# Performance work log

Measured on AMD Instinct MI355X. Metric: run time of the kernel, lower is better.

Reference implementation:

```python
import jax, jax.numpy as jnp
import numpy as np

MAX_THRESHOLD = 0.25  # init kwarg
B, S, D, E = 8, 4096, 512, 8


def setup_inputs() -> dict:
    key = jax.random.key(0)
    ks = jax.random.split(key, 5)
    scale = 1.0 / np.sqrt(D)
    return {
        "inputs": jax.random.normal(ks[0], (B, S, D), dtype=jnp.float32),
        "W_gate": jax.random.normal(ks[1], (D, E), dtype=jnp.float32) * scale,
        "b_gate": jnp.zeros((E,), dtype=jnp.float32),
        "W_thr": jax.random.normal(ks[2], (D, 1), dtype=jnp.float32) * scale,
        "b_thr": jnp.zeros((1,), dtype=jnp.float32),
        "W_exp": jax.random.normal(ks[3], (E, D, D), dtype=jnp.float32) * scale,
        "b_exp": jnp.zeros((E, D), dtype=jnp.float32),
    }


def reference(inputs, W_gate, b_gate, W_thr, b_thr, W_exp, b_exp):
    d = inputs.shape[-1]
    x = inputs.reshape(-1, d)  # [T, D]
    # gating
    gate_logits = jax.nn.softmax(x @ W_gate + b_gate, axis=-1)          # [T, E]
    thresholds = jax.nn.sigmoid(x @ W_thr + b_thr) * MAX_THRESHOLD      # [T, 1]
    adapted = gate_logits - thresholds                                  # [T, E]
    selected = (adapted >= 0).astype(x.dtype)                           # [T, E]
    weights = adapted * selected                                        # [T, E]
    wsum = jnp.sum(weights, axis=-1, keepdims=True)
    wsum = jnp.where(wsum == 0, jnp.ones_like(wsum), wsum)
    weights = weights / wsum
    # dense-equivalent of gather->expert->scatter (weights are 0 where unselected)
    ex_out = jnp.einsum('td,edf->etf', x, W_exp) + b_exp[:, None, :]    # [E, T, D]
    results = jnp.einsum('etf,te->tf', ex_out, weights)                 # [T, D]
    return results.reshape(inputs.shape[:-1] + (results.shape[-1],))
```

## Files before the change

### kernel.cpp

```cpp
#include <hip/hip_runtime.h>


#define T_TOKENS 32768
#define DDIM 512
#define KDIM 4096
#define SLOTB 16384
#define SLOTA 16384

typedef __attribute__((ext_vector_type(8))) short short8;
typedef __attribute__((ext_vector_type(4))) float floatx4;
typedef __bf16 bf16x2 __attribute__((ext_vector_type(2)));

__device__ __forceinline__ unsigned short f2bf(float f) {
    unsigned int u = __float_as_uint(f);
    u += 0x7FFFu + ((u >> 16) & 1u);
    return (unsigned short)(u >> 16);
}

__device__ __forceinline__ unsigned int pk2(float a, float b) {
#if __has_builtin(__builtin_amdgcn_cvt_pk_bf16_f32)
    bf16x2 v = __builtin_amdgcn_cvt_pk_bf16_f32(a, b);
    return __builtin_bit_cast(unsigned int, v);
#else
    return (unsigned int)f2bf(a) | ((unsigned int)f2bf(b) << 16);
#endif
}

__device__ __forceinline__ void async_copy16(const void* g, void* l) {
    __builtin_amdgcn_global_load_lds(
        (const __attribute__((address_space(1))) void*)g,
        (__attribute__((address_space(3))) void*)l, 16, 0, 0);
}

__device__ __forceinline__ unsigned int scale_pair(unsigned int u, float w) {
    float lo = __uint_as_float(u << 16) * w;
    float hi = __uint_as_float(u & 0xFFFF0000u) * w;
    return pk2(lo, hi);
}

__global__ __launch_bounds__(256) void gating_cvt_bt(
    const float* __restrict__ x, const float* __restrict__ Wg,
    const float* __restrict__ bg, const float* __restrict__ Wt,
    const float* __restrict__ bt, float* __restrict__ wbuf,
    unsigned short* __restrict__ Xbf,
    const float* __restrict__ Wexp, unsigned short* __restrict__ Bt)
{
    __shared__ float sW[512 * 12];
    const int tid = threadIdx.x;

    if (blockIdx.x >= 512) {
        float(*tile)[65] = (float(*)[65])sW;
        const int bb = blockIdx.x - 512;
        const int k0 = (bb & 63) * 64;
        const int n0 = (bb >> 6) * 64;
        const int r = tid >> 4, cq = tid & 15;
#pragma unroll
        for (int p = 0; p < 4; ++p) {
            const int rr = p * 16 + r;
            const float4 v = *(const float4*)(Wexp + (size_t)(k0 + rr) * 512 + n0 + cq * 4);
            tile[rr][cq * 4 + 0] = v.x;
            tile[rr][cq * 4 + 1] = v.y;
            tile[rr][cq * 4 + 2] = v.z;
            tile[rr][cq * 4 + 3] = v.w;
        }
        __syncthreads();
        const int rn = tid >> 2;
        const int kq = tid & 3;
        alignas(16) unsigned short buf[16];
#pragma unroll
        for (int j = 0; j < 16; ++j) buf[j] = f2bf(tile[kq * 16 + j][rn]);
        unsigned short* dst = Bt + (size_t)(n0 + rn) * KDIM + k0 + kq * 16;
        *(uint4*)(dst) = *(const uint4*)(buf);
        *(uint4*)(dst + 8) = *(const uint4*)(buf + 8);
        return;
    }

    for (int i = tid; i < 512 * 9; i += 256) {
        int d = i / 9, e = i - d * 9;
        sW[d * 12 + e] = (e < 8) ? Wg[d * 8 + e] : Wt[d];
    }
    __syncthreads();

    const int t = blockIdx.x * 64 + (tid >> 2);
    const int q = tid & 3;
    float g[9];
#pragma unroll
    for (int e = 0; e < 9; ++e) g[e] = 0.f;

    const float4* xr = (const float4*)(x + (size_t)t * 512 + q * 128);
    for (int i = 0; i < 32; ++i) {
        float4 v = xr[i];
        float xv[4] = {v.x, v.y, v.z, v.w};
        const float* wp = &sW[(q * 128 + i * 4) * 12];
#pragma unroll
        for (int c = 0; c < 4; ++c) {
            const float* w = wp + c * 12;
#pragma unroll
            for (int e = 0; e < 9; ++e) g[e] = fmaf(xv[c], w[e], g[e]);
        }
    }
#pragma unroll
    for (int e = 0; e < 9; ++e) {
        g[e] += __shfl_xor(g[e], 1);
        g[e] += __shfl_xor(g[e], 2);
    }
    if (q == 0) {
#pragma unroll
        for (int e = 0; e < 8; ++e) g[e] += bg[e];
        g[8] += bt[0];
        float m = g[0];
#pragma unroll
        for (int e = 1; e < 8; ++e) m = fmaxf(m, g[e]);
        float s = 0.f;
        float p[8];
#pragma unroll
        for (int e = 0; e < 8; ++e) { p[e] = __expf(g[e] - m); s += p[e]; }
        const float inv = 1.f / s;
        const float thr = 0.25f / (1.f + __expf(-g[8]));
        float w8[8];
        float ws = 0.f;
#pragma unroll
        for (int e = 0; e < 8; ++e) {
            float a = p[e] * inv - thr;
            w8[e] = a > 0.f ? a : 0.f;
            ws += w8[e];
        }
        if (ws == 0.f) ws = 1.f;
        const float invw = 1.f / ws;
        float4 o0, o1;
        o0.x = w8[0] * invw; o0.y = w8[1] * invw; o0.z = w8[2] * invw; o0.w = w8[3] * invw;
        o1.x = w8[4] * invw; o1.y = w8[5] * invw; o1.z = w8[6] * invw; o1.w = w8[7] * invw;
        float4* op = (float4*)(wbuf + (size_t)t * 8);
        op[0] = o0;
        op[1] = o1;
    }

    const size_t base = (size_t)blockIdx.x * 64 * 512;
    const float4* xs = (const float4*)(x + base);
    uint2* xd = (uint2*)(Xbf + base);
#pragma unroll 4
    for (int it = 0; it < 32; ++it) {
        float4 v = xs[it * 256 + tid];
        uint2 pk;
        pk.x = pk2(v.x, v.y);
        pk.y = pk2(v.z, v.w);
        xd[it * 256 + tid] = pk;
    }
}

__global__ __launch_bounds__(512, 2) void moe_gemm(
    const unsigned short* __restrict__ Xbf, const float* __restrict__ wbuf,
    const float* __restrict__ bexp, const unsigned short* __restrict__ Bt,
    float* __restrict__ out)
{
    __shared__ alignas(16) unsigned short Bs[3 * SLOTB];
    __shared__ alignas(16) unsigned short As[SLOTA];
    __shared__ float sWbT[8 * 256];

    const int tid = threadIdx.x;
    const int wave = tid >> 6;
    const int lane = tid & 63;
    const int wm = wave >> 2;
    const int wn = wave & 3;
    const int lm = lane & 15;
    const int lq = lane >> 4;
    const int brow = lane >> 3;
    const int cg = (lane & 7) ^ brow;
    const int c8 = tid & 7;
    const int r0 = tid >> 3;
    const int swzA = ((c8 ^ (r0 & 7)) << 3);

    const int lin = blockIdx.x;
    const int g = lin & 7;
    const int j_ = lin >> 3;
    const int t0 = (g * 16 + (j_ >> 1)) * 256;
    const int n0 = (j_ & 1) * 256;

    {
        const int row = tid & 255, pr = tid >> 8;
        const float4 w4 = *(const float4*)(wbuf + (size_t)(t0 + row) * 8 + pr * 4);
        sWbT[(pr * 4 + 0) * 256 + row] = w4.x;
        sWbT[(pr * 4 + 1) * 256 + row] = w4.y;
        sWbT[(pr * 4 + 2) * 256 + row] = w4.z;
        sWbT[(pr * 4 + 3) * 256 + row] = w4.w;
    }

#define STAGE_B(s_, slot_, i0, i1)                                              \
    {                                                                           \
        const int k0_ = (s_) << 6;                                              \
        _Pragma("unroll")                                                       \
        for (int i = (i0); i < (i1); ++i)                                       \
            async_copy16(Bt + (size_t)(n0 + wave * 32 + i * 8 + brow) * KDIM + k0_ + cg * 8, \
                         Bs + (slot_) * SLOTB + (wave * 32 + i * 8) * 64);      \
    }
#define LOADA_ISSUE(s_)                                                         \
    {                                                                           \
        const int d0_ = ((s_) & 7) << 6;                                        \
        _Pragma("unroll")                                                       \
        for (int m = 0; m < 4; ++m)                                             \
            ar[m] = *(const uint4*)(Xbf + (size_t)(t0 + r0 + m * 64) * 512 + d0_ + c8 * 8); \
    }
#define ASCALE_WRITE(s_)                                                        \
    {                                                                           \
        const int e1 = (s_) >> 3;                                               \
        _Pragma("unroll")                                                       \
        for (int m = 0; m < 4; ++m) {                                           \
            const float w = sWbT[e1 * 256 + r0 + m * 64];                       \
            uint4 o;                                                            \
            o.x = scale_pair(ar[m].x, w);                                       \
            o.y = scale_pair(ar[m].y, w);                                       \
            o.z = scale_pair(ar[m].z, w);                                       \
            o.w = scale_pair(ar[m].w, w);                                       \
            *(uint4*)(As + (r0 + m * 64) * 64 + swzA) = o;                      \
        }                                                                       \
    }
#define READ_A(ih)                                                              \
    {                                                                           \
        _Pragma("unroll")                                                       \
        for (int ii = 0; ii < 4; ++ii)                                          \
            _Pragma("unroll")                                                   \
            for (int kk = 0; kk < 2; ++kk) {                                    \
                const int row = wm * 128 + ((ih) * 4 + ii) * 16 + lm;           \
                const int ch = kk * 4 + lq;                                     \
                af[ii][kk] = *(const short8*)(As + row * 64 + ((ch ^ (row & 7)) << 3)); \
            }                                                                   \
    }
#define READ_B(q_, dst)                                                         \
    {                                                                           \
        _Pragma("unroll")                                                       \
        for (int jj = 0; jj < 2; ++jj)                                          \
            _Pragma("unroll")                                                   \
            for (int kk = 0; kk < 2; ++kk) {                                    \
                const int row = wn * 64 + ((q_) * 2 + jj) * 16 + lm;            \
                const int ch = kk * 4 + lq;                                     \
                dst[jj][kk] = *(const short8*)(Bb + row * 64 + ((ch ^ (row & 7)) << 3)); \
            }                                                                   \
    }
#define MFMA_Q(ih, q_, bq)                                                      \
    {                                                                           \
        __builtin_amdgcn_s_setprio(1);                                          \
        _Pragma("unroll")                                                       \
        for (int ii = 0; ii < 4; ++ii)                                          \
            _Pragma("unroll")                                                   \
            for (int jj = 0; jj < 2; ++jj)                                      \
                _Pragma("unroll")                                               \
                for (int kk = 0; kk < 2; ++kk)                                  \
                    acc[(ih) * 4 + ii][(q_) * 2 + jj] =                         \
                        __builtin_amdgcn_mfma_f32_16x16x32_bf16(                \
                            af[ii][kk], bq[jj][kk], acc[(ih) * 4 + ii][(q_) * 2 + jj], 0, 0, 0); \
        __builtin_amdgcn_s_setprio(0);                                          \
    }

    floatx4 acc[8][4];
#pragma unroll
    for (int i = 0; i < 8; ++i)
#pragma unroll
        for (int j = 0; j < 4; ++j) acc[i][j] = (floatx4){0.f, 0.f, 0.f, 0.f};

    uint4 ar[4];

    LOADA_ISSUE(0);
    STAGE_B(0, 0, 0, 4);
    STAGE_B(1, 1, 0, 4);
    asm volatile("s_waitcnt vmcnt(8)" ::: "memory");
    ASCALE_WRITE(0);
    asm volatile("s_waitcnt vmcnt(4) lgkmcnt(0)" ::: "memory");
    __builtin_amdgcn_s_barrier();

    int sB = 0;
    for (int s = 0; s < 64; ++s) {
        const int sB1 = (sB == 2) ? 0 : sB + 1;
        const int sB2 = (sB == 0) ? 2 : sB - 1;
        const unsigned short* Bb = Bs + sB * SLOTB;
        short8 af[4][2], b0[2][2], b1[2][2];

        READ_A(0);
        READ_B(0, b0);
        if (s < 63) LOADA_ISSUE(s + 1);
        __builtin_amdgcn_s_barrier();
        MFMA_Q(0, 0, b0);
        __builtin_amdgcn_s_barrier();

        READ_B(1, b1);
        if (s < 62) STAGE_B(s + 2, sB2, 0, 2);
        __builtin_amdgcn_s_barrier();
        MFMA_Q(0, 1, b1);
        __builtin_amdgcn_s_barrier();

        READ_A(1);
        if (s < 62) STAGE_B(s + 2, sB2, 2, 4);
        __builtin_amdgcn_s_barrier();
        MFMA_Q(1, 1, b1);
        __builtin_amdgcn_s_barrier();

        if (s < 62) {
            asm volatile("s_waitcnt vmcnt(4)" ::: "memory");
        } else if (s == 62) {
            asm volatile("s_waitcnt vmcnt(0)" ::: "memory");
        }
        if (s < 63) ASCALE_WRITE(s + 1);
        READ_B(0, b0);
        __builtin_amdgcn_s_barrier();
        MFMA_Q(1, 0, b0);
        asm volatile("s_waitcnt lgkmcnt(0)" ::: "memory");
        __builtin_amdgcn_s_barrier();

        sB = sB1;
    }

    float bc[4][8];
#pragma unroll
    for (int j = 0; j < 4; ++j) {
        const int col = n0 + wn * 64 + j * 16 + lm;
#pragma unroll
        for (int e = 0; e < 8; ++e) bc[j][e] = bexp[e * 512 + col];
    }
#pragma unroll
    for (int i = 0; i < 8; ++i)
#pragma unroll
        for (int r = 0; r < 4; ++r) {
            const int rowl = wm * 128 + i * 16 + lq * 4 + r;
            const float4 w0 = *(const float4*)(wbuf + (size_t)(t0 + rowl) * 8);
            const float4 w1 = *(const float4*)(wbuf + (size_t)(t0 + rowl) * 8 + 4);
            float* op = out + (size_t)(t0 + rowl) * 512 + n0 + wn * 64 + lm;
#pragma unroll
            for (int j = 0; j < 4; ++j) {
                float bias = w0.x * bc[j][0];
                bias = fmaf(w0.y, bc[j][1], bias);
                bias = fmaf(w0.z, bc[j][2], bias);
                bias = fmaf(w0.w, bc[j][3], bias);
                bias = fmaf(w1.x, bc[j][4], bias);
                bias = fmaf(w1.y, bc[j][5], bias);
                bias = fmaf(w1.z, bc[j][6], bias);
                bias = fmaf(w1.w, bc[j][7], bias);
                op[j * 16] = acc[i][j][r] + bias;
            }
        }
#undef STAGE_B
#undef LOADA_ISSUE
#undef ASCALE_WRITE
#undef READ_A
#undef READ_B
#undef MFMA_Q
}

extern "C" void kernel_launch(void* const* d_in, const int* in_sizes, int n_in,
                              void* d_out, int out_size, void* d_ws, size_t ws_size,
                              hipStream_t stream) {
    const float* x   = (const float*)d_in[0];
    const float* Wg  = (const float*)d_in[1];
    const float* bg  = (const float*)d_in[2];
    const float* Wt  = (const float*)d_in[3];
    const float* bt  = (const float*)d_in[4];
    const float* Wex = (const float*)d_in[5];
    const float* bex = (const float*)d_in[6];
    float* out = (float*)d_out;

    unsigned short* Xbf = (unsigned short*)d_ws;
    unsigned short* Bt  = (unsigned short*)((char*)d_ws + (size_t)T_TOKENS * DDIM * 2);
    float* wbuf = (float*)((char*)d_ws + (size_t)T_TOKENS * DDIM * 2
                                       + (size_t)DDIM * KDIM * 2);

    gating_cvt_bt<<<1024, 256, 0, stream>>>(x, Wg, bg, Wt, bt, wbuf, Xbf, Wex, Bt);
    moe_gemm<<<256, 512, 0, stream>>>(Xbf, wbuf, bex, Bt, out);
}
```

Before: 286.7 us.

## Fuse gating dot-products with bf16 conversion using register-resident gate weights

Rewrites the gating part of the preprocessing kernel so each wave handles 16 whole tokens. Each lane holds its 8-column slice of the gate and threshold weights in registers, and the x row is read once to produce both the bf16 copy and the gate logits. This removes the second global read of x, the shared-memory staging of Wg and the block barrier. In exchange it adds a full 64-lane butterfly reduction across nine values per token, and 72+ registers of weights per lane may lower occupancy.

```diff
diff --git a/kernel.cpp b/kernel.cpp
--- a/kernel.cpp
+++ b/kernel.cpp
@@ -45,11 +45,10 @@
     unsigned short* __restrict__ Xbf,
     const float* __restrict__ Wexp, unsigned short* __restrict__ Bt)
 {
-    __shared__ float sW[512 * 12];
     const int tid = threadIdx.x;
 
     if (blockIdx.x >= 512) {
-        float(*tile)[65] = (float(*)[65])sW;
+        __shared__ float tile[64][65];
         const int bb = blockIdx.x - 512;
         const int k0 = (bb & 63) * 64;
         const int n0 = (bb >> 6) * 64;
@@ -75,76 +74,93 @@
         return;
     }
 
-    for (int i = tid; i < 512 * 9; i += 256) {
-        int d = i / 9, e = i - d * 9;
-        sW[d * 12 + e] = (e < 8) ? Wg[d * 8 + e] : Wt[d];
-    }
-    __syncthreads();
-
-    const int t = blockIdx.x * 64 + (tid >> 2);
-    const int q = tid & 3;
-    float g[9];
-#pragma unroll
-    for (int e = 0; e < 9; ++e) g[e] = 0.f;
-
-    const float4* xr = (const float4*)(x + (size_t)t * 512 + q * 128);
-    for (int i = 0; i < 32; ++i) {
-        float4 v = xr[i];
-        float xv[4] = {v.x, v.y, v.z, v.w};
-        const float* wp = &sW[(q * 128 + i * 4) * 12];
-#pragma unroll
-        for (int c = 0; c < 4; ++c) {
-            const float* w = wp + c * 12;
-#pragma unroll
-            for (int e = 0; e < 9; ++e) g[e] = fmaf(xv[c], w[e], g[e]);
-        }
-    }
-#pragma unroll
-    for (int e = 0; e < 9; ++e) {
-        g[e] += __shfl_xor(g[e], 1);
-        g[e] += __shfl_xor(g[e], 2);
-    }
-    if (q == 0) {
-#pragma unroll
-        for (int e = 0; e < 8; ++e) g[e] += bg[e];
-        g[8] += bt[0];
-        float m = g[0];
-#pragma unroll
-        for (int e = 1; e < 8; ++e) m = fmaxf(m, g[e]);
-        float s = 0.f;
-        float p[8];
-#pragma unroll
-        for (int e = 0; e < 8; ++e) { p[e] = __expf(g[e] - m); s += p[e]; }
-        const float inv = 1.f / s;
-        const float thr = 0.25f / (1.f + __expf(-g[8]));
-        float w8[8];
-        float ws = 0.f;
-#pragma unroll
-        for (int e = 0; e < 8; ++e) {
-            float a = p[e] * inv - thr;
-            w8[e] = a > 0.f ? a : 0.f;
-            ws += w8[e];
-        }
-        if (ws == 0.f) ws = 1.f;
-        const float invw = 1.f / ws;
-        float4 o0, o1;
-        o0.x = w8[0] * invw; o0.y = w8[1] * invw; o0.z = w8[2] * invw; o0.w = w8[3] * invw;
-        o1.x = w8[4] * invw; o1.y = w8[5] * invw; o1.z = w8[6] * invw; o1.w = w8[7] * invw;
-        float4* op = (float4*)(wbuf + (size_t)t * 8);
-        op[0] = o0;
-        op[1] = o1;
-    }
-
-    const size_t base = (size_t)blockIdx.x * 64 * 512;
-    const float4* xs = (const float4*)(x + base);
-    uint2* xd = (uint2*)(Xbf + base);
-#pragma unroll 4
-    for (int it = 0; it < 32; ++it) {
-        float4 v = xs[it * 256 + tid];
-        uint2 pk;
-        pk.x = pk2(v.x, v.y);
-        pk.y = pk2(v.z, v.w);
-        xd[it * 256 + tid] = pk;
+    const int wv = tid >> 6;
+    const int lane = tid & 63;
+
+    float4 wg[16];
+    {
+        const float4* wgp = (const float4*)(Wg + lane * 64);
+#pragma unroll
+        for (int c = 0; c < 16; ++c) wg[c] = wgp[c];
+    }
+    const float4 wt0 = *(const float4*)(Wt + lane * 8);
+    const float4 wt1 = *(const float4*)(Wt + lane * 8 + 4);
+    const float bgv[8] = {bg[0], bg[1], bg[2], bg[3], bg[4], bg[5], bg[6], bg[7]};
+    const float btv = bt[0];
+
+    for (int it = 0; it < 16; ++it) {
+        const int t = blockIdx.x * 64 + wv * 16 + it;
+        const float* xp = x + (size_t)t * 512 + lane * 8;
+        const float4 a0 = *(const float4*)(xp);
+        const float4 a1 = *(const float4*)(xp + 4);
+
+        uint2 pk0, pk1;
+        pk0.x = pk2(a0.x, a0.y);
+        pk0.y = pk2(a0.z, a0.w);
+        pk1.x = pk2(a1.x, a1.y);
+        pk1.y = pk2(a1.z, a1.w);
+        uint2* xd = (uint2*)(Xbf + (size_t)t * 512 + lane * 8);
+        xd[0] = pk0;
+        xd[1] = pk1;
+
+        const float xv[8] = {a0.x, a0.y, a0.z, a0.w, a1.x, a1.y, a1.z, a1.w};
+        const float wtv[8] = {wt0.x, wt0.y, wt0.z, wt0.w, wt1.x, wt1.y, wt1.z, wt1.w};
+        float g[9];
+#pragma unroll
+        for (int e = 0; e < 9; ++e) g[e] = 0.f;
+#pragma unroll
+        for (int j = 0; j < 8; ++j) {
+            const float4 wlo = wg[j * 2];
+            const float4 whi = wg[j * 2 + 1];
+            g[0] = fmaf(xv[j], wlo.x, g[0]);
+            g[1] = fmaf(xv[j], wlo.y, g[1]);
+            g[2] = fmaf(xv[j], wlo.z, g[2]);
+            g[3] = fmaf(xv[j], wlo.w, g[3]);
+            g[4] = fmaf(xv[j], whi.x, g[4]);
+            g[5] = fmaf(xv[j], whi.y, g[5]);
+            g[6] = fmaf(xv[j], whi.z, g[6]);
+            g[7] = fmaf(xv[j], whi.w, g[7]);
+            g[8] = fmaf(xv[j], wtv[j], g[8]);
+        }
+#pragma unroll
+        for (int e = 0; e < 9; ++e) {
+            g[e] += __shfl_xor(g[e], 1);
+            g[e] += __shfl_xor(g[e], 2);
+            g[e] += __shfl_xor(g[e], 4);
+            g[e] += __shfl_xor(g[e], 8);
+            g[e] += __shfl_xor(g[e], 16);
+            g[e] += __shfl_xor(g[e], 32);
+        }
+        if (lane == 0) {
+#pragma unroll
+            for (int e = 0; e < 8; ++e) g[e] += bgv[e];
+            g[8] += btv;
+            float m = g[0];
+#pragma unroll
+            for (int e = 1; e < 8; ++e) m = fmaxf(m, g[e]);
+            float s = 0.f;
+            float p[8];
+#pragma unroll
+            for (int e = 0; e < 8; ++e) { p[e] = __expf(g[e] - m); s += p[e]; }
+            const float inv = 1.f / s;
+            const float thr = 0.25f / (1.f + __expf(-g[8]));
+            float w8[8];
+            float ws = 0.f;
+#pragma unroll
+            for (int e = 0; e < 8; ++e) {
+                float a = p[e] * inv - thr;
+                w8[e] = a > 0.f ? a : 0.f;
+                ws += w8[e];
+            }
+            if (ws == 0.f) ws = 1.f;
+            const float invw = 1.f / ws;
+            float4 o0, o1;
+            o0.x = w8[0] * invw; o0.y = w8[1] * invw; o0.z = w8[2] * invw; o0.w = w8[3] * invw;
+            o1.x = w8[4] * invw; o1.y = w8[5] * invw; o1.z = w8[6] * invw; o1.w = w8[7] * invw;
+            float4* op = (float4*)(wbuf + (size_t)t * 8);
+            op[0] = o0;
+            op[1] = o1;
+        }
     }
 }
 
```

After: 282.7 us. About the same (-1.4%).
